# Optimization experiments

Hardware: AMD Instinct MI355X
Metric: run time of the kernel (lower is better)

Reference implementation:

```python
import jax, jax.numpy as jnp
import numpy as np

NUM_CLASSES = 1000
ATTR_EMBED_DIM = 128
DIM_Z = 512
DIM_G = 1024
INIT_STD = 0.2
SCALING = 1.0
REGULARIZE_G = 1.0
EPS = 1e-6


def setup_inputs() -> dict:
    key = jax.random.key(0)
    ks = jax.random.split(key, 6)
    B, C, P = 8, 4, 512
    qz = jax.random.normal(ks[0], (B, C, P, DIM_Z), dtype=jnp.float32)
    attr_idx = jax.random.randint(ks[1], (B,), 0, NUM_CLASSES)
    W_base = INIT_STD * jax.random.normal(ks[2], (DIM_G, DIM_Z), dtype=jnp.float32)
    embed_table = jax.random.normal(ks[3], (NUM_CLASSES, ATTR_EMBED_DIM), dtype=jnp.float32)
    lim_u = 1.0 / np.sqrt(ATTR_EMBED_DIM)
    Wu = jax.random.uniform(ks[4], (DIM_G, ATTR_EMBED_DIM), minval=-lim_u, maxval=lim_u, dtype=jnp.float32)
    Wv = jax.random.uniform(ks[5], (DIM_Z, ATTR_EMBED_DIM), minval=-lim_u, maxval=lim_u, dtype=jnp.float32)
    return {"qz": qz, "attr_idx": attr_idx, "W_base": W_base,
            "embed_table": embed_table, "Wu": Wu, "Wv": Wv}


def _abs_norm(x):
    # relu in fp32, then L1-normalize along last dim (torch F.normalize p=1)
    x = jax.nn.relu(x.astype(jnp.float32))
    denom = jnp.maximum(jnp.sum(jnp.abs(x), axis=-1, keepdims=True), EPS)
    return x / denom


def reference(qz, attr_idx, W_base, embed_table, Wu, Wv):
    a_emb = embed_table[attr_idx]                 # [B, E]
    u = a_emb @ Wu.T                              # [B, G]
    v = a_emb @ Wv.T                              # [B, D]
    # Per-sample rank-1 perturbed factor: W = W_base + u \otimes v  -> [B, G, D]
    W = W_base[None, :, :] + u[:, :, None] * v[:, None, :]
    qg = jnp.einsum('bcpd,bgd->bcpg', qz, W) * SCALING
    qg = _abs_norm(qg / REGULARIZE_G)
    return jnp.einsum('bcpg,bgd->bcpd', qg, W) * SCALING
```

## Files before the change

kernel.cpp:

```cpp
#include <hip/hip_runtime.h>
#include <hip/hip_bf16.h>

#define BATCH   8
#define MROWS   2048
#define MTOT    16384
#define DIM_Z   512
#define DIM_G   1024
#define EDIM    128
#define EPS     1e-6f
#define BK      64

typedef unsigned short u16;
typedef unsigned int   u32;
typedef __attribute__((ext_vector_type(8))) short bf16x8;
typedef __attribute__((ext_vector_type(4))) float f32x4;

__device__ __forceinline__ u16 f2b(float f) {
    u32 x = __float_as_uint(f);
    u32 r = x + 0x7fffu + ((x >> 16) & 1u);
    return (u16)(r >> 16);
}

__device__ __forceinline__ u32 cvtpk(float lo, float hi) {
    u32 r;
    asm("v_cvt_pk_bf16_f32 %0, %1, %2" : "=v"(r) : "v"(lo), "v"(hi));
    return r;
}

#define GLD16(gsrc, ldst) __builtin_amdgcn_global_load_lds( \
    (const __attribute__((address_space(1))) unsigned int*)(gsrc), \
    (__attribute__((address_space(3))) unsigned int*)(ldst), 16, 0, 0)

#define MEMFENCE() asm volatile("" ::: "memory")

__global__ void uv_kernel(const float* __restrict__ emb, const int* __restrict__ idx,
                          const float* __restrict__ Wu, const float* __restrict__ Wv,
                          float* __restrict__ u, float* __restrict__ v,
                          float* __restrict__ rsum) {
    __shared__ float a[EDIM];
    int b = blockIdx.y;
    int t = threadIdx.x;
    if (blockIdx.x == 0)
        for (int i = t; i < MROWS; i += 256) rsum[(size_t)b * MROWS + i] = 0.f;
    if (t < EDIM) a[t] = emb[(size_t)idx[b] * EDIM + t];
    __syncthreads();
    int tx = t & 31, ty = t >> 5;
    int oBase = blockIdx.x * 256;
    for (int o0 = 0; o0 < 256; o0 += 8) {
        int o = oBase + o0 + ty;
        const float* wrow = (o < DIM_G) ? (Wu + (size_t)o * EDIM)
                                        : (Wv + (size_t)(o - DIM_G) * EDIM);
        float s = 0.f;
#pragma unroll
        for (int q = 0; q < 4; ++q) s += a[q * 32 + tx] * wrow[q * 32 + tx];
        s += __shfl_xor(s, 1, 64);
        s += __shfl_xor(s, 2, 64);
        s += __shfl_xor(s, 4, 64);
        s += __shfl_xor(s, 8, 64);
        s += __shfl_xor(s, 16, 64);
        if (tx == 0) {
            if (o < DIM_G) u[b * DIM_G + o] = s;
            else           v[b * DIM_Z + (o - DIM_G)] = s;
        }
    }
}

__global__ void wpack_kernel(const float* __restrict__ Wbase,
                             const float* __restrict__ u, const float* __restrict__ v,
                             u16* __restrict__ W, u16* __restrict__ WT) {
    __shared__ u16 tile[32][33];
    int h = blockIdx.x;
    int b = h & 7, t8 = h >> 3;
    int d0 = (t8 & 15) * 32, g0 = (t8 >> 4) * 32;
    int tx = threadIdx.x, ty = threadIdx.y;
    float vb = v[b * DIM_Z + d0 + tx];
#pragma unroll
    for (int j = 0; j < 4; ++j) {
        int g = g0 + ty + j * 8;
        u16 h16 = f2b(Wbase[(size_t)g * DIM_Z + d0 + tx] + u[b * DIM_G + g] * vb);
        W[((size_t)b * DIM_G + g) * DIM_Z + d0 + tx] = h16;
        tile[ty + j * 8][tx] = h16;
    }
    __syncthreads();
#pragma unroll
    for (int j = 0; j < 4; ++j)
        WT[((size_t)b * DIM_Z + d0 + ty + j * 8) * DIM_G + g0 + tx] =
            tile[tx][ty + j * 8];
}

__global__ __launch_bounds__(256, 2)
void gemm1(const float* __restrict__ qz, const u16* __restrict__ Wall,
           u16* __restrict__ qg, float* __restrict__ rsum) {
    const int N = DIM_G, K = DIM_Z;
    __shared__ u16 As[128 * BK];
    __shared__ u16 Bs[256 * BK];

    int h = blockIdx.x;
    int xcd = h & 7, idx = h >> 3;
    int tile = xcd * 64 + idx;
    int mBase = (tile >> 2) * 128;
    int nBase = (tile & 3) * 256;
    int b = mBase >> 11;

    int tid  = threadIdx.x;
    int lane = tid & 63, wid = tid >> 6;
    int wm = wid >> 1, wn = wid & 1;
    int lr = lane & 15, lg = lane >> 4;

    f32x4 acc[4][8] = {};

    int sRow = tid >> 3;
    int sC   = tid & 7;
    int cw   = sC ^ (sRow & 7);
    const float* aSrc = qz + (size_t)(mBase + sRow) * K + sC * 8;
    const u16*   bSrc = Wall + (size_t)b * DIM_G * DIM_Z
                             + (size_t)(nBase + sRow) * K + cw * 8;

    float4 alo[2][4], ahi[2][4];
#pragma unroll
    for (int r = 0; r < 4; ++r) {
        const float* g = aSrc + (size_t)r * 32 * K;
        alo[0][r] = *(const float4*)g;
        ahi[0][r] = *(const float4*)(g + 4);
    }

#pragma unroll
    for (int t = 0; t < 8; ++t) {
        const int cur = t & 1, nxt = cur ^ 1;
        __builtin_amdgcn_s_barrier();
        MEMFENCE();
#pragma unroll
        for (int r = 0; r < 8; ++r)
            GLD16(bSrc + (size_t)r * 32 * K + t * BK, &Bs[(r * 256 + wid * 64) * 8]);
        if (t < 7) {
#pragma unroll
            for (int r = 0; r < 4; ++r) {
                const float* g = aSrc + (size_t)r * 32 * K + (t + 1) * BK;
                alo[nxt][r] = *(const float4*)g;
                ahi[nxt][r] = *(const float4*)(g + 4);
            }
        }
#pragma unroll
        for (int r = 0; r < 4; ++r) {
            uint4 q;
            q.x = cvtpk(alo[cur][r].x, alo[cur][r].y);
            q.y = cvtpk(alo[cur][r].z, alo[cur][r].w);
            q.z = cvtpk(ahi[cur][r].x, ahi[cur][r].y);
            q.w = cvtpk(ahi[cur][r].z, ahi[cur][r].w);
            *(uint4*)&As[(r * 32 + sRow) * BK + cw * 8] = q;
        }
        if (t < 7) asm volatile("s_waitcnt vmcnt(8) lgkmcnt(0)" ::: "memory");
        else       asm volatile("s_waitcnt vmcnt(0) lgkmcnt(0)" ::: "memory");
        __builtin_amdgcn_s_barrier();
        MEMFENCE();
#pragma unroll
        for (int ks = 0; ks < 2; ++ks) {
            bf16x8 af[4], bfr[8];
#pragma unroll
            for (int mi = 0; mi < 4; ++mi) {
                int row = wm * 64 + mi * 16 + lr;
                int cq  = (ks * 4 + lg) ^ (row & 7);
                af[mi] = *(const bf16x8*)&As[row * BK + cq * 8];
            }
#pragma unroll
            for (int ni = 0; ni < 8; ++ni) {
                int row = wn * 128 + ni * 16 + lr;
                int cq  = (ks * 4 + lg) ^ (row & 7);
                bfr[ni] = *(const bf16x8*)&Bs[row * BK + cq * 8];
            }
            __builtin_amdgcn_s_setprio(1);
#pragma unroll
            for (int mi = 0; mi < 4; ++mi)
#pragma unroll
                for (int ni = 0; ni < 8; ++ni)
                    acc[mi][ni] = __builtin_amdgcn_mfma_f32_16x16x32_bf16(
                        af[mi], bfr[ni], acc[mi][ni], 0, 0, 0);
            __builtin_amdgcn_s_setprio(0);
        }
        MEMFENCE();
    }

    int mw = mBase + wm * 64, nw = nBase + wn * 128;
#pragma unroll
    for (int mi = 0; mi < 4; ++mi)
#pragma unroll
        for (int r = 0; r < 4; ++r) {
            int m = mw + mi * 16 + lg * 4 + r;
            float vals[8];
            float s = 0.f;
#pragma unroll
            for (int ni = 0; ni < 8; ++ni) {
                vals[ni] = fmaxf(acc[mi][ni][r], 0.f);
                s += vals[ni];
            }
#pragma unroll
            for (int ni = 0; ni < 8; ++ni)
                qg[(size_t)m * N + nw + ni * 16 + lr] = f2b(vals[ni]);
            s += __shfl_xor(s, 1, 64);
            s += __shfl_xor(s, 2, 64);
            s += __shfl_xor(s, 4, 64);
            s += __shfl_xor(s, 8, 64);
            if (lr == 0) atomicAdd(&rsum[m], s);
        }
}

__global__ __launch_bounds__(256, 4)
void gemm2(const u16* __restrict__ qg, const u16* __restrict__ WTall,
           const float* __restrict__ rsum, float* __restrict__ out) {
    const int N = DIM_Z, K = DIM_G;
    __shared__ u16 As[128 * BK];
    __shared__ u16 Bs[128 * BK];

    int h = blockIdx.x;
    int xcd = h & 7, idx = h >> 3;
    int tile = xcd * 64 + idx;
    int mBase = (tile >> 2) * 128;
    int nBase = (tile & 3) * 128;
    int b = mBase >> 11;

    int tid  = threadIdx.x;
    int lane = tid & 63, wid = tid >> 6;
    int wm = wid >> 1, wn = wid & 1;
    int lr = lane & 15, lg = lane >> 4;

    f32x4 acc[4][4] = {};

    int sRow = tid >> 3;
    int cw   = (tid & 7) ^ (sRow & 7);
    const u16* aSrc = qg + (size_t)(mBase + sRow) * K + cw * 8;
    const u16* bSrc = WTall + (size_t)b * DIM_Z * DIM_G
                            + (size_t)(nBase + sRow) * K + cw * 8;

    for (int kt = 0; kt < K; kt += BK) {
        __syncthreads();
#pragma unroll
        for (int r = 0; r < 4; ++r) {
            GLD16(aSrc + (size_t)r * 32 * K + kt, &As[(r * 256 + wid * 64) * 8]);
            GLD16(bSrc + (size_t)r * 32 * K + kt, &Bs[(r * 256 + wid * 64) * 8]);
        }
        __syncthreads();
#pragma unroll
        for (int ks = 0; ks < 2; ++ks) {
            bf16x8 af[4], bfr[4];
#pragma unroll
            for (int mi = 0; mi < 4; ++mi) {
                int row = wm * 64 + mi * 16 + lr;
                int cq  = (ks * 4 + lg) ^ (row & 7);
                af[mi] = *(const bf16x8*)&As[row * BK + cq * 8];
            }
#pragma unroll
            for (int ni = 0; ni < 4; ++ni) {
                int row = wn * 64 + ni * 16 + lr;
                int cq  = (ks * 4 + lg) ^ (row & 7);
                bfr[ni] = *(const bf16x8*)&Bs[row * BK + cq * 8];
            }
            __builtin_amdgcn_s_setprio(1);
#pragma unroll
            for (int mi = 0; mi < 4; ++mi)
#pragma unroll
                for (int ni = 0; ni < 4; ++ni)
                    acc[mi][ni] = __builtin_amdgcn_mfma_f32_16x16x32_bf16(
                        af[mi], bfr[ni], acc[mi][ni], 0, 0, 0);
            __builtin_amdgcn_s_setprio(0);
        }
    }

    int mw = mBase + wm * 64, nw = nBase + wn * 64;
#pragma unroll
    for (int mi = 0; mi < 4; ++mi)
#pragma unroll
        for (int r = 0; r < 4; ++r) {
            int m = mw + mi * 16 + lg * 4 + r;
            float inv = 1.f / fmaxf(rsum[m], EPS);
#pragma unroll
            for (int ni = 0; ni < 4; ++ni)
                __builtin_nontemporal_store(acc[mi][ni][r] * inv,
                    &out[(size_t)m * N + nw + ni * 16 + lr]);
        }
}

extern "C" void kernel_launch(void* const* d_in, const int* in_sizes, int n_in,
                              void* d_out, int out_size, void* d_ws, size_t ws_size,
                              hipStream_t stream) {
    const float* qz    = (const float*)d_in[0];
    const int*   attr  = (const int*)d_in[1];
    const float* Wbase = (const float*)d_in[2];
    const float* emb   = (const float*)d_in[3];
    const float* Wu    = (const float*)d_in[4];
    const float* Wv    = (const float*)d_in[5];
    float* out = (float*)d_out;

    char* ws = (char*)d_ws;
    size_t off = 0;
    auto alloc = [&](size_t bytes) -> void* {
        void* p = ws + off;
        off = (off + bytes + 255) & ~(size_t)255;
        return p;
    };
    float* u    = (float*)alloc((size_t)BATCH * DIM_G * 4);
    float* v    = (float*)alloc((size_t)BATCH * DIM_Z * 4);
    float* rsum = (float*)alloc((size_t)MTOT * 4);
    u16*   W    = (u16*)  alloc((size_t)BATCH * DIM_G * DIM_Z * 2);
    u16*   WT   = (u16*)  alloc((size_t)BATCH * DIM_G * DIM_Z * 2);
    u16*   qg   = (u16*)  alloc((size_t)MTOT * DIM_G * 2);
    if (off > ws_size) return;

    uv_kernel<<<dim3(6, BATCH), dim3(256), 0, stream>>>(emb, attr, Wu, Wv, u, v, rsum);

    wpack_kernel<<<dim3(4096), dim3(32, 8), 0, stream>>>(Wbase, u, v, W, WT);

    gemm1<<<dim3(512), dim3(256), 0, stream>>>(qz, W, qg, rsum);

    gemm2<<<dim3(512), dim3(256), 0, stream>>>(qg, WT, rsum, out);
}
```

Measured before the change: 79.46 us.

## Fuse u/v projection into W packing kernel and loop batches per block

Merges the attribute projection kernel into the weight packing kernel. Each of 512 blocks now owns a 32x32 (g,d) tile, computes the needed slices of u and v for every batch in-block, loads W_base once, and writes bf16 W and WT for all 8 batches. This removes one kernel launch and the u/v round trip through global memory, and reuses the W_base tile across batches. In exchange each block redundantly recomputes its u/v slices and runs fewer, longer serialized blocks with extra barriers.

Result: faster. 67.92 us (-14.5%).

```diff
diff --git a/kernel.cpp b/kernel.cpp
--- a/kernel.cpp
+++ b/kernel.cpp
@@ -33,59 +33,60 @@
 
 #define MEMFENCE() asm volatile("" ::: "memory")
 
-__global__ void uv_kernel(const float* __restrict__ emb, const int* __restrict__ idx,
-                          const float* __restrict__ Wu, const float* __restrict__ Wv,
-                          float* __restrict__ u, float* __restrict__ v,
-                          float* __restrict__ rsum) {
-    __shared__ float a[EDIM];
-    int b = blockIdx.y;
-    int t = threadIdx.x;
-    if (blockIdx.x == 0)
-        for (int i = t; i < MROWS; i += 256) rsum[(size_t)b * MROWS + i] = 0.f;
-    if (t < EDIM) a[t] = emb[(size_t)idx[b] * EDIM + t];
-    __syncthreads();
-    int tx = t & 31, ty = t >> 5;
-    int oBase = blockIdx.x * 256;
-    for (int o0 = 0; o0 < 256; o0 += 8) {
-        int o = oBase + o0 + ty;
-        const float* wrow = (o < DIM_G) ? (Wu + (size_t)o * EDIM)
-                                        : (Wv + (size_t)(o - DIM_G) * EDIM);
+__global__ void wpack_uv(const float* __restrict__ Wbase,
+                         const float* __restrict__ emb, const int* __restrict__ idx,
+                         const float* __restrict__ Wu, const float* __restrict__ Wv,
+                         u16* __restrict__ W, u16* __restrict__ WT,
+                         float* __restrict__ rsum) {
+    __shared__ float a_sh[EDIM];
+    __shared__ float us[32], vs[32];
+    __shared__ u16 tile[32][33];
+
+    int h = blockIdx.x;
+    int d0 = (h & 15) * 32, g0 = (h >> 4) * 32;
+    int tx = threadIdx.x, ty = threadIdx.y;
+    int tid = ty * 32 + tx;
+
+    if (h < 64)
+        for (int i = tid; i < 256; i += 256) rsum[h * 256 + i] = 0.f;
+
+    float base[4];
+#pragma unroll
+    for (int j = 0; j < 4; ++j)
+        base[j] = Wbase[(size_t)(g0 + ty + j * 8) * DIM_Z + d0 + tx];
+
+    int slot = tid >> 2, q = tid & 3;
+    const float* wrow = (slot < 32) ? (Wu + (size_t)(g0 + slot) * EDIM)
+                                    : (Wv + (size_t)(d0 + slot - 32) * EDIM);
+
+    for (int b = 0; b < BATCH; ++b) {
+        if (tid < EDIM) a_sh[tid] = emb[(size_t)idx[b] * EDIM + tid];
+        __syncthreads();
         float s = 0.f;
 #pragma unroll
-        for (int q = 0; q < 4; ++q) s += a[q * 32 + tx] * wrow[q * 32 + tx];
+        for (int i = 0; i < 32; ++i) s += a_sh[q * 32 + i] * wrow[q * 32 + i];
         s += __shfl_xor(s, 1, 64);
         s += __shfl_xor(s, 2, 64);
-        s += __shfl_xor(s, 4, 64);
-        s += __shfl_xor(s, 8, 64);
-        s += __shfl_xor(s, 16, 64);
-        if (tx == 0) {
-            if (o < DIM_G) u[b * DIM_G + o] = s;
-            else           v[b * DIM_Z + (o - DIM_G)] = s;
-        }
+        if (q == 0) {
+            if (slot < 32) us[slot] = s;
+            else           vs[slot - 32] = s;
+        }
+        __syncthreads();
+        float vb = vs[tx];
+#pragma unroll
+        for (int j = 0; j < 4; ++j) {
+            int g = g0 + ty + j * 8;
+            u16 h16 = f2b(base[j] + us[ty + j * 8] * vb);
+            W[((size_t)b * DIM_G + g) * DIM_Z + d0 + tx] = h16;
+            tile[ty + j * 8][tx] = h16;
+        }
+        __syncthreads();
+#pragma unroll
+        for (int j = 0; j < 4; ++j)
+            WT[((size_t)b * DIM_Z + d0 + ty + j * 8) * DIM_G + g0 + tx] =
+                tile[tx][ty + j * 8];
+        __syncthreads();
     }
-}
-
-__global__ void wpack_kernel(const float* __restrict__ Wbase,
-                             const float* __restrict__ u, const float* __restrict__ v,
-                             u16* __restrict__ W, u16* __restrict__ WT) {
-    __shared__ u16 tile[32][33];
-    int h = blockIdx.x;
-    int b = h & 7, t8 = h >> 3;
-    int d0 = (t8 & 15) * 32, g0 = (t8 >> 4) * 32;
-    int tx = threadIdx.x, ty = threadIdx.y;
-    float vb = v[b * DIM_Z + d0 + tx];
-#pragma unroll
-    for (int j = 0; j < 4; ++j) {
-        int g = g0 + ty + j * 8;
-        u16 h16 = f2b(Wbase[(size_t)g * DIM_Z + d0 + tx] + u[b * DIM_G + g] * vb);
-        W[((size_t)b * DIM_G + g) * DIM_Z + d0 + tx] = h16;
-        tile[ty + j * 8][tx] = h16;
-    }
-    __syncthreads();
-#pragma unroll
-    for (int j = 0; j < 4; ++j)
-        WT[((size_t)b * DIM_Z + d0 + ty + j * 8) * DIM_G + g0 + tx] =
-            tile[tx][ty + j * 8];
 }
 
 __global__ __launch_bounds__(256, 2)
@@ -297,17 +298,14 @@
         off = (off + bytes + 255) & ~(size_t)255;
         return p;
     };
-    float* u    = (float*)alloc((size_t)BATCH * DIM_G * 4);
-    float* v    = (float*)alloc((size_t)BATCH * DIM_Z * 4);
     float* rsum = (float*)alloc((size_t)MTOT * 4);
     u16*   W    = (u16*)  alloc((size_t)BATCH * DIM_G * DIM_Z * 2);
     u16*   WT   = (u16*)  alloc((size_t)BATCH * DIM_G * DIM_Z * 2);
     u16*   qg   = (u16*)  alloc((size_t)MTOT * DIM_G * 2);
     if (off > ws_size) return;
 
-    uv_kernel<<<dim3(6, BATCH), dim3(256), 0, stream>>>(emb, attr, Wu, Wv, u, v, rsum);
-
-    wpack_kernel<<<dim3(4096), dim3(32, 8), 0, stream>>>(Wbase, u, v, W, WT);
+    wpack_uv<<<dim3(512), dim3(32, 8), 0, stream>>>(
+        Wbase, emb, attr, Wu, Wv, W, WT, rsum);
 
     gemm1<<<dim3(512), dim3(256), 0, stream>>>(qz, W, qg, rsum);
 
```
